# Performance work log

Hardware: AMD Instinct MI355X
Metric: run time of the kernel (lower is better)

Reference implementation:

```python
import jax, jax.numpy as jnp
import numpy as np

N = 50000      # nodes
E = 400000     # edges
IN = 128       # in_dim == emb_dim (residual requires equality)
POS = 64       # pos_in_dim
EMB = 128
LN_EPS = 1e-5


def _ln(x, g, b):
    m = jnp.mean(x, axis=-1, keepdims=True)
    v = jnp.mean((x - m) ** 2, axis=-1, keepdims=True)
    return (x - m) / jnp.sqrt(v + LN_EPS) * g + b


def _gin(x, src, dst, eps, W1, b1, g1, be1, W2, b2):
    # GINConv: mlp((1+eps)*x + sum_{j in N(i)} x_j)
    agg = jax.ops.segment_sum(x[src], dst, num_segments=x.shape[0])
    h = (1.0 + eps) * x + agg
    h = jax.nn.relu(_ln(h @ W1 + b1, g1, be1))
    return h @ W2 + b2


def setup_inputs() -> dict:
    key = jax.random.key(0)
    ks = jax.random.split(key, 8)
    x = jax.random.normal(ks[0], (N, IN), jnp.float32)
    pos = jax.random.normal(ks[1], (N, POS), jnp.float32)
    edge_index = jax.random.randint(ks[2], (2, E), 0, N)
    d = IN + POS
    f32 = jnp.float32
    W1 = (jax.random.normal(ks[3], (d, EMB), f32) / np.sqrt(d))
    W2 = (jax.random.normal(ks[4], (EMB, EMB), f32) / np.sqrt(EMB))
    W1p = (jax.random.normal(ks[5], (POS, EMB), f32) / np.sqrt(POS))
    W2p = (jax.random.normal(ks[6], (EMB, EMB), f32) / np.sqrt(EMB))
    z = jnp.zeros((EMB,), f32)
    o = jnp.ones((EMB,), f32)
    return {
        "x": x, "pos": pos, "edge_index": edge_index,
        "eps": jnp.zeros((), f32), "W1": W1, "b1": z, "g1": o, "be1": z,
        "W2": W2, "b2": z, "ln_g": o, "ln_b": z,
        "epsp": jnp.zeros((), f32), "W1p": W1p, "b1p": z, "g1p": o, "be1p": z,
        "W2p": W2p, "b2p": z, "lnp_g": o, "lnp_b": z,
    }


def reference(x, pos, edge_index, eps, W1, b1, g1, be1, W2, b2, ln_g, ln_b,
              epsp, W1p, b1p, g1p, be1p, W2p, b2p, lnp_g, lnp_b):
    src, dst = edge_index[0], edge_index[1]
    node_feats = jnp.concatenate([x, pos], axis=-1)  # [N, IN+POS]
    h = jax.nn.relu(_ln(_gin(node_feats, src, dst, eps, W1, b1, g1, be1, W2, b2), ln_g, ln_b))
    p = jax.nn.relu(_ln(_gin(pos, src, dst, epsp, W1p, b1p, g1p, be1p, W2p, b2p), lnp_g, lnp_b))
    # dropout is identity in eval mode (model_drop_ratio applied only when training)
    h = h + x  # add_residual=True
    return (h, p)
```

## Files before the change

### kernel.cpp

```cpp
#include <hip/hip_runtime.h>

#define NN    50000
#define NPAD  50048
#define HB    391
#define EE    400000
#define IND   128
#define POSD  64
#define DD    192
#define EMBD  128
#define LNEPS 1e-5f
#define CAP   32

typedef __attribute__((ext_vector_type(8))) short bf16x8;
typedef __attribute__((ext_vector_type(4))) unsigned short u16x4;
typedef __attribute__((ext_vector_type(4))) float f32x4;
typedef unsigned short ushort_t;
typedef unsigned int uint_t;

#define MFMA16 __builtin_amdgcn_mfma_f32_16x16x32_bf16

__device__ inline ushort_t f2bf(float f) {
  union { float f; unsigned u; } v; v.f = f;
  unsigned r = (v.u + 0x7FFFu + ((v.u >> 16) & 1u)) >> 16;
  return (ushort_t)r;
}
__device__ inline float bf2f(unsigned u) {
  union { unsigned u; float f; } v; v.u = u << 16;
  return v.f;
}

__global__ __launch_bounds__(256) void cat_k(
    const float* __restrict__ x, const float* __restrict__ pos,
    ushort_t* __restrict__ cat) {
  int id  = blockIdx.x * 256 + threadIdx.x;
  int n   = id / 24, sub = id - n * 24;
  bf16x8 o = (bf16x8){0, 0, 0, 0, 0, 0, 0, 0};
  if (n < NN) {
    const float* src = (sub < 16) ? (x + (size_t)n * IND + sub * 8)
                                  : (pos + (size_t)n * POSD + (sub - 16) * 8);
    f32x4 v0 = *(const f32x4*)(src);
    f32x4 v1 = *(const f32x4*)(src + 4);
#pragma unroll
    for (int i = 0; i < 4; ++i) {
      o[i]     = (short)f2bf(v0[i]);
      o[i + 4] = (short)f2bf(v1[i]);
    }
  }
  *(bf16x8*)(cat + (size_t)n * DD + sub * 8) = o;
}

__global__ __launch_bounds__(256) void fillv_k(
    const int* __restrict__ ei, int* __restrict__ cnt, int* __restrict__ csr) {
  int e0 = (blockIdx.x * 256 + threadIdx.x) * 4;
  if (e0 >= EE) return;
  int4 s = *(const int4*)(ei + e0);
  int4 d = *(const int4*)(ei + EE + e0);
  int i0 = atomicAdd(&cnt[d.x], 1);
  int i1 = atomicAdd(&cnt[d.y], 1);
  int i2 = atomicAdd(&cnt[d.z], 1);
  int i3 = atomicAdd(&cnt[d.w], 1);
  if (i0 < CAP) csr[(size_t)d.x * CAP + i0] = s.x;
  if (i1 < CAP) csr[(size_t)d.y * CAP + i1] = s.y;
  if (i2 < CAP) csr[(size_t)d.z * CAP + i2] = s.z;
  if (i3 < CAP) csr[(size_t)d.w * CAP + i3] = s.w;
}

__global__ __launch_bounds__(256) void wconv_k(
    const float* __restrict__ W1, const float* __restrict__ W2,
    const float* __restrict__ W1p, const float* __restrict__ W2p,
    ushort_t* __restrict__ wt) {
  int t = blockIdx.x * 256 + threadIdx.x;
  if (t < 24576) {
    int c = t / 192, k = t % 192;
    wt[t] = f2bf(W1[k * EMBD + c]);
  } else if (t < 40960) {
    int q = t - 24576; int c = q / 128, k = q % 128;
    wt[t] = f2bf(W2[k * EMBD + c]);
  } else if (t < 49152) {
    int q = t - 40960; int c = q / 64, k = q % 64;
    wt[t] = f2bf(W1p[k * EMBD + c]);
  } else {
    int q = t - 49152; int c = q / 128, k = q % 128;
    wt[t] = f2bf(W2p[k * EMBD + c]);
  }
}

__global__ __launch_bounds__(256) void gather2_k(
    const ushort_t* __restrict__ cat, const int* __restrict__ cnt,
    const int* __restrict__ csr,
    const float* __restrict__ epsv, const float* __restrict__ epspv,
    ushort_t* __restrict__ h0, ushort_t* __restrict__ p0) {
  const int lane = threadIdx.x & 63;
  const int wv   = threadIdx.x >> 6;
  const int half = lane >> 5;
  const int l2   = lane & 31;
  const int n    = blockIdx.x * 8 + wv * 2 + half;

  int deg = 0;
  if (n < NN) { deg = cnt[n]; if (deg > CAP) deg = CAP; }
  int idx = (l2 < deg) ? csr[(size_t)n * CAP + l2] : NN;

  float a0 = 0.f, a1 = 0.f, a2 = 0.f, a3 = 0.f, a4 = 0.f, a5 = 0.f;
  for (int t = 0; t < deg; t += 8) {
    int s[8];
#pragma unroll
    for (int k = 0; k < 8; ++k) s[k] = __shfl(idx, half * 32 + t + k);
    u16x4 u[8]; uint_t v[8];
#pragma unroll
    for (int k = 0; k < 8; ++k) {
      int sk = (t + k < CAP) ? s[k] : NN;
      const ushort_t* r = cat + (size_t)sk * DD;
      u[k] = *(const u16x4*)(r + l2 * 4);
      v[k] = *(const uint_t*)(r + 128 + l2 * 2);
    }
#pragma unroll
    for (int k = 0; k < 8; ++k) {
      a0 += bf2f(u[k][0]); a1 += bf2f(u[k][1]);
      a2 += bf2f(u[k][2]); a3 += bf2f(u[k][3]);
      a4 += bf2f(v[k] & 0xffffu); a5 += bf2f(v[k] >> 16);
    }
  }

  const float e1  = 1.0f + epsv[0];
  const float ep1 = 1.0f + epspv[0];
  const ushort_t* self = cat + (size_t)n * DD;
  u16x4 su = *(const u16x4*)(self + l2 * 4);
  uint_t sv = *(const uint_t*)(self + 128 + l2 * 2);

  u16x4 o;
  o[0] = f2bf(fmaf(e1, bf2f(su[0]), a0));
  o[1] = f2bf(fmaf(e1, bf2f(su[1]), a1));
  o[2] = f2bf(fmaf(e1, bf2f(su[2]), a2));
  o[3] = f2bf(fmaf(e1, bf2f(su[3]), a3));
  *(u16x4*)(h0 + (size_t)n * DD + l2 * 4) = o;

  float p4 = bf2f(sv & 0xffffu), p5 = bf2f(sv >> 16);
  uint_t oh = (uint_t)f2bf(fmaf(e1, p4, a4)) |
              ((uint_t)f2bf(fmaf(e1, p5, a5)) << 16);
  *(uint_t*)(h0 + (size_t)n * DD + 128 + l2 * 2) = oh;
  uint_t op = (uint_t)f2bf(fmaf(ep1, p4, a4)) |
              ((uint_t)f2bf(fmaf(ep1, p5, a5)) << 16);
  *(uint_t*)(p0 + (size_t)n * POSD + l2 * 2) = op;
}

__device__ inline void ln_epi_T(f32x4 (&acc)[8][2],
                                const float* __restrict__ bias,
                                const float* __restrict__ gam,
                                const float* __restrict__ bet, int g) {
  f32x4 bv[8], gv[8], bev[8];
#pragma unroll
  for (int nt = 0; nt < 8; ++nt) {
    bv[nt]  = *(const f32x4*)(bias + nt * 16 + g * 4);
    gv[nt]  = *(const f32x4*)(gam  + nt * 16 + g * 4);
    bev[nt] = *(const f32x4*)(bet  + nt * 16 + g * 4);
  }
#pragma unroll
  for (int mt = 0; mt < 2; ++mt) {
    float s = 0.f, sq = 0.f;
#pragma unroll
    for (int nt = 0; nt < 8; ++nt)
#pragma unroll
      for (int r = 0; r < 4; ++r) {
        float v = acc[nt][mt][r] + bv[nt][r];
        acc[nt][mt][r] = v;
        s += v; sq += v * v;
      }
    s  += __shfl_xor(s, 16);  sq += __shfl_xor(sq, 16);
    s  += __shfl_xor(s, 32);  sq += __shfl_xor(sq, 32);
    float mean = s * (1.0f / 128.0f);
    float var  = sq * (1.0f / 128.0f) - mean * mean;
    float rstd = rsqrtf(var + LNEPS);
#pragma unroll
    for (int nt = 0; nt < 8; ++nt)
#pragma unroll
      for (int r = 0; r < 4; ++r)
        acc[nt][mt][r] = fmaxf(
            fmaf((acc[nt][mt][r] - mean) * rstd, gv[nt][r], bev[nt][r]), 0.f);
  }
}

__device__ inline void act_write_T(char* act, f32x4 (&acc)[8][2], int g, int c0) {
#pragma unroll
  for (int mt = 0; mt < 2; ++mt) {
    int lr = mt * 16 + c0;
    int sw = (lr & 7) << 4;
#pragma unroll
    for (int nt = 0; nt < 8; ++nt) {
      u16x4 o;
#pragma unroll
      for (int r = 0; r < 4; ++r) o[r] = f2bf(acc[nt][mt][r]);
      *(u16x4*)(act + lr * 256 + ((nt * 32 + g * 8) ^ sw)) = o;
    }
  }
}

__device__ inline void stage_w(const ushort_t* __restrict__ src, char* dst,
                               int rowbytes, int chunks, int tid) {
  int cpr = rowbytes >> 4;
  for (int i = tid; i < chunks; i += 256) {
    int row  = i / cpr;
    int colb = (i - row * cpr) << 4;
    *(bf16x8*)(dst + row * rowbytes + (colb ^ ((row & 7) << 4))) =
        *(const bf16x8*)(src + (size_t)i * 8);
  }
}

__global__ __launch_bounds__(256) void mlp_k(
    const ushort_t* __restrict__ h0, const ushort_t* __restrict__ p0,
    const ushort_t* __restrict__ wt,
    const float* __restrict__ b1, const float* __restrict__ g1,
    const float* __restrict__ be1,
    const float* __restrict__ b2, const float* __restrict__ lng,
    const float* __restrict__ lnb,
    const float* __restrict__ b1p, const float* __restrict__ g1p,
    const float* __restrict__ be1p,
    const float* __restrict__ b2p, const float* __restrict__ lnpg,
    const float* __restrict__ lnpb,
    const float* __restrict__ x, float* __restrict__ out) {
  __shared__ __align__(16) char smem[81920];
  const int tid  = threadIdx.x;
  const int lane = tid & 63;
  const int wv   = tid >> 6;
  const int g    = lane >> 4;
  const int c0   = lane & 15;
  const int bid  = blockIdx.x;
  char* act = smem + 49152 + wv * 8192;

  f32x4 acc[8][2];

  if (bid < HB) {
    const int m0 = bid * 128;
    stage_w(wt, smem, 384, 3072, tid);
    bf16x8 a0[6], a1[6];
    const size_t r0 = (size_t)(m0 + wv * 32 + c0) * DD;
    const size_t r1 = r0 + (size_t)16 * DD;
#pragma unroll
    for (int ks = 0; ks < 6; ++ks) {
      a0[ks] = *(const bf16x8*)(h0 + r0 + ks * 32 + g * 8);
      a1[ks] = *(const bf16x8*)(h0 + r1 + ks * 32 + g * 8);
    }
    __syncthreads();

#pragma unroll
    for (int nt = 0; nt < 8; ++nt)
#pragma unroll
      for (int mt = 0; mt < 2; ++mt) acc[nt][mt] = (f32x4){0.f, 0.f, 0.f, 0.f};
#pragma unroll
    for (int ks = 0; ks < 6; ++ks)
#pragma unroll
      for (int nt = 0; nt < 8; ++nt) {
        int wrow = nt * 16 + c0;
        bf16x8 w = *(const bf16x8*)(smem + wrow * 384 +
                                    ((ks * 64 + g * 16) ^ ((wrow & 7) << 4)));
        acc[nt][0] = MFMA16(w, a0[ks], acc[nt][0], 0, 0, 0);
        acc[nt][1] = MFMA16(w, a1[ks], acc[nt][1], 0, 0, 0);
      }
    ln_epi_T(acc, b1, g1, be1, g);
    act_write_T(act, acc, g, c0);
    __syncthreads();
    stage_w(wt + 24576, smem, 256, 2048, tid);
    __syncthreads();

#pragma unroll
    for (int nt = 0; nt < 8; ++nt)
#pragma unroll
      for (int mt = 0; mt < 2; ++mt) acc[nt][mt] = (f32x4){0.f, 0.f, 0.f, 0.f};
#pragma unroll
    for (int ks = 0; ks < 4; ++ks) {
      bf16x8 am[2];
#pragma unroll
      for (int mt = 0; mt < 2; ++mt) {
        int lr = mt * 16 + c0;
        am[mt] = *(const bf16x8*)(act + lr * 256 +
                                  ((ks * 64 + g * 16) ^ ((lr & 7) << 4)));
      }
#pragma unroll
      for (int nt = 0; nt < 8; ++nt) {
        int wrow = nt * 16 + c0;
        bf16x8 w = *(const bf16x8*)(smem + wrow * 256 +
                                    ((ks * 64 + g * 16) ^ ((wrow & 7) << 4)));
        acc[nt][0] = MFMA16(w, am[0], acc[nt][0], 0, 0, 0);
        acc[nt][1] = MFMA16(w, am[1], acc[nt][1], 0, 0, 0);
      }
    }
    ln_epi_T(acc, b2, lng, lnb, g);
#pragma unroll
    for (int mt = 0; mt < 2; ++mt) {
      int node = m0 + wv * 32 + mt * 16 + c0;
      if (node < NN) {
#pragma unroll
        for (int nt = 0; nt < 8; ++nt) {
          int f0 = nt * 16 + g * 4;
          f32x4 xr = *(const f32x4*)(x + (size_t)node * IND + f0);
          f32x4 o;
#pragma unroll
          for (int r = 0; r < 4; ++r) o[r] = acc[nt][mt][r] + xr[r];
          *(f32x4*)(out + (size_t)node * EMBD + f0) = o;
        }
      }
    }
  } else {
    const int m0 = (bid - HB) * 128;
    stage_w(wt + 40960, smem, 128, 1024, tid);
    stage_w(wt + 49152, smem + 16384, 256, 2048, tid);
    bf16x8 a0[2], a1[2];
    const size_t r0 = (size_t)(m0 + wv * 32 + c0) * POSD;
    const size_t r1 = r0 + (size_t)16 * POSD;
#pragma unroll
    for (int ks = 0; ks < 2; ++ks) {
      a0[ks] = *(const bf16x8*)(p0 + r0 + ks * 32 + g * 8);
      a1[ks] = *(const bf16x8*)(p0 + r1 + ks * 32 + g * 8);
    }
    __syncthreads();

#pragma unroll
    for (int nt = 0; nt < 8; ++nt)
#pragma unroll
      for (int mt = 0; mt < 2; ++mt) acc[nt][mt] = (f32x4){0.f, 0.f, 0.f, 0.f};
#pragma unroll
    for (int ks = 0; ks < 2; ++ks)
#pragma unroll
      for (int nt = 0; nt < 8; ++nt) {
        int wrow = nt * 16 + c0;
        bf16x8 w = *(const bf16x8*)(smem + wrow * 128 +
                                    ((ks * 64 + g * 16) ^ ((wrow & 7) << 4)));
        acc[nt][0] = MFMA16(w, a0[ks], acc[nt][0], 0, 0, 0);
        acc[nt][1] = MFMA16(w, a1[ks], acc[nt][1], 0, 0, 0);
      }
    ln_epi_T(acc, b1p, g1p, be1p, g);
    act_write_T(act, acc, g, c0);

#pragma unroll
    for (int nt = 0; nt < 8; ++nt)
#pragma unroll
      for (int mt = 0; mt < 2; ++mt) acc[nt][mt] = (f32x4){0.f, 0.f, 0.f, 0.f};
#pragma unroll
    for (int ks = 0; ks < 4; ++ks) {
      bf16x8 am[2];
#pragma unroll
      for (int mt = 0; mt < 2; ++mt) {
        int lr = mt * 16 + c0;
        am[mt] = *(const bf16x8*)(act + lr * 256 +
                                  ((ks * 64 + g * 16) ^ ((lr & 7) << 4)));
      }
#pragma unroll
      for (int nt = 0; nt < 8; ++nt) {
        int wrow = nt * 16 + c0;
        bf16x8 w = *(const bf16x8*)(smem + 16384 + wrow * 256 +
                                    ((ks * 64 + g * 16) ^ ((wrow & 7) << 4)));
        acc[nt][0] = MFMA16(w, am[0], acc[nt][0], 0, 0, 0);
        acc[nt][1] = MFMA16(w, am[1], acc[nt][1], 0, 0, 0);
      }
    }
    ln_epi_T(acc, b2p, lnpg, lnpb, g);
#pragma unroll
    for (int mt = 0; mt < 2; ++mt) {
      int node = m0 + wv * 32 + mt * 16 + c0;
      if (node < NN) {
#pragma unroll
        for (int nt = 0; nt < 8; ++nt) {
          int f0 = nt * 16 + g * 4;
          f32x4 o;
#pragma unroll
          for (int r = 0; r < 4; ++r) o[r] = acc[nt][mt][r];
          *(f32x4*)(out + (size_t)NN * EMBD + (size_t)node * EMBD + f0) = o;
        }
      }
    }
  }
}

extern "C" void kernel_launch(void* const* d_in, const int* in_sizes, int n_in,
                              void* d_out, int out_size, void* d_ws, size_t ws_size,
                              hipStream_t stream) {
  const float* x    = (const float*)d_in[0];
  const float* pos  = (const float*)d_in[1];
  const int*   ei   = (const int*)d_in[2];
  const float* eps  = (const float*)d_in[3];
  const float* W1   = (const float*)d_in[4];
  const float* b1   = (const float*)d_in[5];
  const float* g1   = (const float*)d_in[6];
  const float* be1  = (const float*)d_in[7];
  const float* W2   = (const float*)d_in[8];
  const float* b2   = (const float*)d_in[9];
  const float* lng  = (const float*)d_in[10];
  const float* lnb  = (const float*)d_in[11];
  const float* epsp = (const float*)d_in[12];
  const float* W1p  = (const float*)d_in[13];
  const float* b1p  = (const float*)d_in[14];
  const float* g1p  = (const float*)d_in[15];
  const float* be1p = (const float*)d_in[16];
  const float* W2p  = (const float*)d_in[17];
  const float* b2p  = (const float*)d_in[18];
  const float* lnpg = (const float*)d_in[19];
  const float* lnpb = (const float*)d_in[20];

  char* ws = (char*)d_ws;
  float* out = (float*)d_out;

  const size_t CATB = (size_t)NPAD * DD * 2;
  const size_t P0B  = (size_t)NPAD * POSD * 2;

  int*      cnt = (int*)ws;
  int*      csr = (int*)(ws + 200000);
  ushort_t* cat = (ushort_t*)(ws + 6600000);
  ushort_t* h0  = (ushort_t*)(ws + 6600000 + CATB);
  ushort_t* p0  = (ushort_t*)(ws + 6600000 + 2 * CATB);
  ushort_t* wt  = (ushort_t*)(ws + 6600000 + 2 * CATB + P0B);

  hipMemsetAsync(cnt, 0, (size_t)NN * sizeof(int), stream);
  cat_k<<<(NPAD * 24) / 256, 256, 0, stream>>>(x, pos, cat);
  fillv_k<<<(EE / 4 + 255) / 256, 256, 0, stream>>>(ei, cnt, csr);
  wconv_k<<<256, 256, 0, stream>>>(W1, W2, W1p, W2p, wt);
  gather2_k<<<NPAD / 8, 256, 0, stream>>>(cat, cnt, csr, eps, epsp, h0, p0);
  mlp_k<<<2 * HB, 256, 0, stream>>>(
      h0, p0, wt, b1, g1, be1, b2, lng, lnb,
      b1p, g1p, be1p, b2p, lnpg, lnpb, x, out);
}
```

Before: 115.5 us.

## Fuse prep kernels into one launch and shrink MLP shared memory footprint

Merges the concat/bf16 conversion, CSR fill and weight transpose kernels into a single block-partitioned prep kernel, cutting two launches and letting the independent work overlap. In the MLP kernel, the per-wave activation buffers now reuse the first-layer weight region and the second-layer weights are staged after layer one finishes, shrinking LDS from 80 KB to 64 KB so more blocks can reside per CU. This adds an extra barrier and moves second-layer weight staging in the pos branch onto the critical path after layer one.

```diff
diff --git a/kernel.cpp b/kernel.cpp
--- a/kernel.cpp
+++ b/kernel.cpp
@@ -11,6 +11,11 @@
 #define LNEPS 1e-5f
 #define CAP   32
 
+#define CAT_B  4692
+#define FILL_B 98
+#define FILLV_B 391
+#define WC_B   256
+
 typedef __attribute__((ext_vector_type(8))) short bf16x8;
 typedef __attribute__((ext_vector_type(4))) unsigned short u16x4;
 typedef __attribute__((ext_vector_type(4))) float f32x4;
@@ -29,59 +34,58 @@
   return v.f;
 }
 
-__global__ __launch_bounds__(256) void cat_k(
+__global__ __launch_bounds__(256) void prep_k(
     const float* __restrict__ x, const float* __restrict__ pos,
-    ushort_t* __restrict__ cat) {
-  int id  = blockIdx.x * 256 + threadIdx.x;
-  int n   = id / 24, sub = id - n * 24;
-  bf16x8 o = (bf16x8){0, 0, 0, 0, 0, 0, 0, 0};
-  if (n < NN) {
-    const float* src = (sub < 16) ? (x + (size_t)n * IND + sub * 8)
-                                  : (pos + (size_t)n * POSD + (sub - 16) * 8);
-    f32x4 v0 = *(const f32x4*)(src);
-    f32x4 v1 = *(const f32x4*)(src + 4);
-#pragma unroll
-    for (int i = 0; i < 4; ++i) {
-      o[i]     = (short)f2bf(v0[i]);
-      o[i + 4] = (short)f2bf(v1[i]);
-    }
-  }
-  *(bf16x8*)(cat + (size_t)n * DD + sub * 8) = o;
-}
-
-__global__ __launch_bounds__(256) void fillv_k(
-    const int* __restrict__ ei, int* __restrict__ cnt, int* __restrict__ csr) {
-  int e0 = (blockIdx.x * 256 + threadIdx.x) * 4;
-  if (e0 >= EE) return;
-  int4 s = *(const int4*)(ei + e0);
-  int4 d = *(const int4*)(ei + EE + e0);
-  int i0 = atomicAdd(&cnt[d.x], 1);
-  int i1 = atomicAdd(&cnt[d.y], 1);
-  int i2 = atomicAdd(&cnt[d.z], 1);
-  int i3 = atomicAdd(&cnt[d.w], 1);
-  if (i0 < CAP) csr[(size_t)d.x * CAP + i0] = s.x;
-  if (i1 < CAP) csr[(size_t)d.y * CAP + i1] = s.y;
-  if (i2 < CAP) csr[(size_t)d.z * CAP + i2] = s.z;
-  if (i3 < CAP) csr[(size_t)d.w * CAP + i3] = s.w;
-}
-
-__global__ __launch_bounds__(256) void wconv_k(
+    const int* __restrict__ ei,
     const float* __restrict__ W1, const float* __restrict__ W2,
     const float* __restrict__ W1p, const float* __restrict__ W2p,
-    ushort_t* __restrict__ wt) {
-  int t = blockIdx.x * 256 + threadIdx.x;
-  if (t < 24576) {
-    int c = t / 192, k = t % 192;
-    wt[t] = f2bf(W1[k * EMBD + c]);
-  } else if (t < 40960) {
-    int q = t - 24576; int c = q / 128, k = q % 128;
-    wt[t] = f2bf(W2[k * EMBD + c]);
-  } else if (t < 49152) {
-    int q = t - 40960; int c = q / 64, k = q % 64;
-    wt[t] = f2bf(W1p[k * EMBD + c]);
+    int* __restrict__ cnt, int* __restrict__ csr,
+    ushort_t* __restrict__ cat, ushort_t* __restrict__ wt) {
+  const int bid = blockIdx.x;
+  if (bid < FILLV_B) {
+    int e0 = (bid * 256 + threadIdx.x) * 4;
+    if (e0 >= EE) return;
+    int4 s = *(const int4*)(ei + e0);
+    int4 d = *(const int4*)(ei + EE + e0);
+    int i0 = atomicAdd(&cnt[d.x], 1);
+    int i1 = atomicAdd(&cnt[d.y], 1);
+    int i2 = atomicAdd(&cnt[d.z], 1);
+    int i3 = atomicAdd(&cnt[d.w], 1);
+    if (i0 < CAP) csr[(size_t)d.x * CAP + i0] = s.x;
+    if (i1 < CAP) csr[(size_t)d.y * CAP + i1] = s.y;
+    if (i2 < CAP) csr[(size_t)d.z * CAP + i2] = s.z;
+    if (i3 < CAP) csr[(size_t)d.w * CAP + i3] = s.w;
+  } else if (bid < FILLV_B + CAT_B) {
+    int id  = (bid - FILLV_B) * 256 + threadIdx.x;
+    int n   = id / 24, sub = id - n * 24;
+    bf16x8 o = (bf16x8){0, 0, 0, 0, 0, 0, 0, 0};
+    if (n < NN) {
+      const float* src = (sub < 16) ? (x + (size_t)n * IND + sub * 8)
+                                    : (pos + (size_t)n * POSD + (sub - 16) * 8);
+      f32x4 v0 = *(const f32x4*)(src);
+      f32x4 v1 = *(const f32x4*)(src + 4);
+#pragma unroll
+      for (int i = 0; i < 4; ++i) {
+        o[i]     = (short)f2bf(v0[i]);
+        o[i + 4] = (short)f2bf(v1[i]);
+      }
+    }
+    *(bf16x8*)(cat + (size_t)n * DD + sub * 8) = o;
   } else {
-    int q = t - 49152; int c = q / 128, k = q % 128;
-    wt[t] = f2bf(W2p[k * EMBD + c]);
+    int t = (bid - FILLV_B - CAT_B) * 256 + threadIdx.x;
+    if (t < 24576) {
+      int c = t / 192, k = t % 192;
+      wt[t] = f2bf(W1[k * EMBD + c]);
+    } else if (t < 40960) {
+      int q = t - 24576; int c = q / 128, k = q % 128;
+      wt[t] = f2bf(W2[k * EMBD + c]);
+    } else if (t < 49152) {
+      int q = t - 40960; int c = q / 64, k = q % 64;
+      wt[t] = f2bf(W1p[k * EMBD + c]);
+    } else {
+      int q = t - 49152; int c = q / 128, k = q % 128;
+      wt[t] = f2bf(W2p[k * EMBD + c]);
+    }
   }
 }
 
@@ -217,14 +221,14 @@
     const float* __restrict__ b2p, const float* __restrict__ lnpg,
     const float* __restrict__ lnpb,
     const float* __restrict__ x, float* __restrict__ out) {
-  __shared__ __align__(16) char smem[81920];
+  __shared__ __align__(16) char smem[65536];
   const int tid  = threadIdx.x;
   const int lane = tid & 63;
   const int wv   = tid >> 6;
   const int g    = lane >> 4;
   const int c0   = lane & 15;
   const int bid  = blockIdx.x;
-  char* act = smem + 49152 + wv * 8192;
+  char* act = smem + wv * 8192;
 
   f32x4 acc[8][2];
 
@@ -256,9 +260,9 @@
         acc[nt][1] = MFMA16(w, a1[ks], acc[nt][1], 0, 0, 0);
       }
     ln_epi_T(acc, b1, g1, be1, g);
+    __syncthreads();
     act_write_T(act, acc, g, c0);
-    __syncthreads();
-    stage_w(wt + 24576, smem, 256, 2048, tid);
+    stage_w(wt + 24576, smem + 32768, 256, 2048, tid);
     __syncthreads();
 
 #pragma unroll
@@ -277,7 +281,7 @@
 #pragma unroll
       for (int nt = 0; nt < 8; ++nt) {
         int wrow = nt * 16 + c0;
-        bf16x8 w = *(const bf16x8*)(smem + wrow * 256 +
+        bf16x8 w = *(const bf16x8*)(smem + 32768 + wrow * 256 +
                                     ((ks * 64 + g * 16) ^ ((wrow & 7) << 4)));
         acc[nt][0] = MFMA16(w, am[0], acc[nt][0], 0, 0, 0);
         acc[nt][1] = MFMA16(w, am[1], acc[nt][1], 0, 0, 0);
@@ -302,7 +306,6 @@
   } else {
     const int m0 = (bid - HB) * 128;
     stage_w(wt + 40960, smem, 128, 1024, tid);
-    stage_w(wt + 49152, smem + 16384, 256, 2048, tid);
     bf16x8 a0[2], a1[2];
     const size_t r0 = (size_t)(m0 + wv * 32 + c0) * POSD;
     const size_t r1 = r0 + (size_t)16 * POSD;
@@ -328,7 +331,10 @@
         acc[nt][1] = MFMA16(w, a1[ks], acc[nt][1], 0, 0, 0);
       }
     ln_epi_T(acc, b1p, g1p, be1p, g);
+    __syncthreads();
     act_write_T(act, acc, g, c0);
+    stage_w(wt + 49152, smem + 32768, 256, 2048, tid);
+    __syncthreads();
 
 #pragma unroll
     for (int nt = 0; nt < 8; ++nt)
@@ -346,7 +352,7 @@
 #pragma unroll
       for (int nt = 0; nt < 8; ++nt) {
         int wrow = nt * 16 + c0;
-        bf16x8 w = *(const bf16x8*)(smem + 16384 + wrow * 256 +
+        bf16x8 w = *(const bf16x8*)(smem + 32768 + wrow * 256 +
                                     ((ks * 64 + g * 16) ^ ((wrow & 7) << 4)));
         acc[nt][0] = MFMA16(w, am[0], acc[nt][0], 0, 0, 0);
         acc[nt][1] = MFMA16(w, am[1], acc[nt][1], 0, 0, 0);
@@ -409,9 +415,8 @@
   ushort_t* wt  = (ushort_t*)(ws + 6600000 + 2 * CATB + P0B);
 
   hipMemsetAsync(cnt, 0, (size_t)NN * sizeof(int), stream);
-  cat_k<<<(NPAD * 24) / 256, 256, 0, stream>>>(x, pos, cat);
-  fillv_k<<<(EE / 4 + 255) / 256, 256, 0, stream>>>(ei, cnt, csr);
-  wconv_k<<<256, 256, 0, stream>>>(W1, W2, W1p, W2p, wt);
+  prep_k<<<FILLV_B + CAT_B + WC_B, 256, 0, stream>>>(
+      x, pos, ei, W1, W2, W1p, W2p, cnt, csr, cat, wt);
   gather2_k<<<NPAD / 8, 256, 0, stream>>>(cat, cnt, csr, eps, epsp, h0, p0);
   mlp_k<<<2 * HB, 256, 0, stream>>>(
       h0, p0, wt, b1, g1, be1, b2, lng, lnb,
```

Result: faster. 111.8 us (-3.2%).
